# Performance work log

Measured on AMD Instinct MI355X. Metric: run time of the kernel, lower is better.

## Reference

```python
import jax, jax.numpy as jnp
import numpy as np

N, E, F_IN, H, C, K = 50000, 800000, 100, 128, 10, 5


def setup_inputs() -> dict:
    key = jax.random.key(0)
    ks = jax.random.split(key, 8)
    x = jax.random.normal(ks[0], (N, F_IN), jnp.float32)
    edge_index = jax.random.randint(ks[1], (2, E), 0, N, dtype=jnp.int64)
    edge_weight = jax.random.uniform(ks[2], (E,), jnp.float32)
    # Hop-wise linear weights: PyG TAGConv holds K+1 bias-free Linears per layer
    W1 = jax.random.normal(ks[3], (K + 1, F_IN, H), jnp.float32) / np.sqrt(F_IN).astype(np.float32)
    b1 = jnp.zeros((H,), jnp.float32)
    W2 = jax.random.normal(ks[4], (K + 1, H, H), jnp.float32) / np.sqrt(H).astype(np.float32)
    b2 = jnp.zeros((H,), jnp.float32)
    W3 = jax.random.normal(ks[5], (K + 1, H, C), jnp.float32) / np.sqrt(H).astype(np.float32)
    b3 = jnp.zeros((C,), jnp.float32)
    return dict(x=x, edge_index=edge_index, edge_weight=edge_weight,
                W1=W1, b1=b1, W2=W2, b2=b2, W3=W3, b3=b3)


def _gcn_norm(row, col, edge_weight, num_nodes):
    # symmetric normalization D^{-1/2} A D^{-1/2}, no self loops (TAGConv default)
    deg = jax.ops.segment_sum(edge_weight, col, num_segments=num_nodes)
    dis = jnp.where(deg > 0, jax.lax.rsqrt(jnp.maximum(deg, 1e-12)), 0.0)
    return dis[row] * edge_weight * dis[col]


def _tagconv(x, row, col, norm, W, b, num_nodes):
    # out = sum_{k=0..K} (A_norm^k x) @ W[k] + b
    out = x @ W[0] + b
    h = x
    for k in range(1, W.shape[0]):
        msg = norm[:, None] * h[row]                       # [E, d] gather
        h = jax.ops.segment_sum(msg, col, num_segments=num_nodes)  # scatter-add
        out = out + h @ W[k]
    return out


def reference(x, edge_index, edge_weight, W1, b1, W2, b2, W3, b3):
    row, col = edge_index[0], edge_index[1]
    norm = _gcn_norm(row, col, edge_weight, N)
    h = jax.nn.elu(_tagconv(x, row, col, norm, W1, b1, N))
    h = jax.nn.elu(_tagconv(h, row, col, norm, W2, b2, N))
    return _tagconv(h, row, col, norm, W3, b3, N)
```

## Files before the change

kernel.cpp:

```cpp
#include <hip/hip_runtime.h>
#include <cstdint>
#include <cstddef>

#define N_NODES 50000
#define N_EDGES 800000
#define F_IN_D 100
#define HDIM 128
#define CDIM 10
#define NCH ((N_NODES + 255) / 256)
#define NLINES 64

typedef unsigned short ushortT;

__device__ __forceinline__ float bf2f(unsigned int b16) {
  return __uint_as_float(b16 << 16);
}
__device__ __forceinline__ unsigned int f2bf(float f) {
  unsigned int u = __float_as_uint(f);
  unsigned int r = u + 0x7FFFu + ((u >> 16) & 1u);
  return r >> 16;
}

struct Args {
  const float* x; const int* ei; const float* ew;
  const float* W1; const float* b1;
  const float* W2; const float* b2;
  const float* W3; const float* b3;
  float* out;
  ushortT* Yall;
  char* A; char* B;
  ushortT* C; ushortT* D;
  int* ptrA; int* pos; int* srcs; float* wsrt;
  int* row32; int* col32; float* deg; float* dis; int* cnt; int* part;
  int* lines;
  int* gbl;
};

__device__ __forceinline__ void gbar(int* lines, int* gbl, int round, int gdim) {
  __syncthreads();
  if (threadIdx.x == 0) {
    __threadfence();
    const int perLine = gdim / NLINES;
    int old = atomicAdd(&lines[(blockIdx.x & (NLINES - 1)) * 32], 1);
    if (old == round * perLine - 1) atomicAdd(gbl, 1);
    while (__hip_atomic_load(gbl, __ATOMIC_ACQUIRE, __HIP_MEMORY_SCOPE_AGENT) < round * NLINES)
      __builtin_amdgcn_s_sleep(8);
    __threadfence();
  }
  __syncthreads();
}

template <int K_DIM, int BMODE, bool XBF, bool OUTBF>
__device__ __forceinline__ void gemm_tile(const void* __restrict__ Xv, const float* __restrict__ W,
                                          const float* __restrict__ bias, bool addb,
                                          void* __restrict__ outv, int ostride, int tile,
                                          float (&xt)[32][68], float (&bt)[32][64]) {
  const int tid = threadIdx.x;
  const int tx = tid & 15;
  const int ty = tid >> 4;
  int n0, c0;
  if (BMODE == 0) { n0 = (tile >> 1) * 64; c0 = (tile & 1) * 64; }
  else            { n0 = tile * 64;        c0 = 0; }
  float acc[4][4];
#pragma unroll
  for (int i = 0; i < 4; ++i)
#pragma unroll
    for (int j = 0; j < 4; ++j) acc[i][j] = 0.f;

  for (int k0 = 0; k0 < K_DIM; k0 += 32) {
#pragma unroll
    for (int i = 0; i < 8; ++i) {
      int idx = tid + i * 256;
      int nl = idx >> 5, kl = idx & 31;
      int nn = n0 + nl, kg = k0 + kl;
      float v = 0.f;
      if (nn < N_NODES && kg < K_DIM) {
        if (XBF) v = bf2f(((const ushortT*)Xv)[(size_t)nn * K_DIM + kg]);
        else     v = ((const float*)Xv)[(size_t)nn * K_DIM + kg];
      }
      xt[kl][nl] = v;
    }
#pragma unroll
    for (int i = 0; i < 8; ++i) {
      int idx = tid + i * 256;
      int kl = idx >> 6, cl = idx & 63;
      int kg = k0 + kl;
      float v = 0.f;
      if (BMODE == 0) {
        if (kg < K_DIM) v = W[(size_t)kg * 128 + c0 + cl];
      } else {
        if (kg < K_DIM && cl < 6 * CDIM)
          v = W[(size_t)(cl / CDIM) * (K_DIM * CDIM) + (size_t)kg * CDIM + (cl % CDIM)];
      }
      bt[kl][cl] = v;
    }
    __syncthreads();
#pragma unroll
    for (int kk = 0; kk < 32; ++kk) {
      float4 xv = *(const float4*)&xt[kk][tx * 4];
      float4 bv = *(const float4*)&bt[kk][ty * 4];
      acc[0][0] += xv.x * bv.x; acc[0][1] += xv.x * bv.y; acc[0][2] += xv.x * bv.z; acc[0][3] += xv.x * bv.w;
      acc[1][0] += xv.y * bv.x; acc[1][1] += xv.y * bv.y; acc[1][2] += xv.y * bv.z; acc[1][3] += xv.y * bv.w;
      acc[2][0] += xv.z * bv.x; acc[2][1] += xv.z * bv.y; acc[2][2] += xv.z * bv.z; acc[2][3] += xv.z * bv.w;
      acc[3][0] += xv.w * bv.x; acc[3][1] += xv.w * bv.y; acc[3][2] += xv.w * bv.z; acc[3][3] += xv.w * bv.w;
    }
    __syncthreads();
  }
#pragma unroll
  for (int i = 0; i < 4; ++i) {
    int nn = n0 + tx * 4 + i;
    if (nn >= N_NODES) continue;
#pragma unroll
    for (int j = 0; j < 4; ++j) {
      int c = c0 + ty * 4 + j;
      if (addb) {
        if (BMODE == 0) acc[i][j] += bias[c];
        else if (c < CDIM) acc[i][j] += bias[c];
      }
    }
    if (OUTBF) {
      uint2 o;
      o.x = f2bf(acc[i][0]) | (f2bf(acc[i][1]) << 16);
      o.y = f2bf(acc[i][2]) | (f2bf(acc[i][3]) << 16);
      *(uint2*)&((ushortT*)outv)[(size_t)nn * ostride + c0 + ty * 4] = o;
    } else {
#pragma unroll
      for (int j = 0; j < 4; ++j)
        ((float*)outv)[(size_t)nn * ostride + c0 + ty * 4 + j] = acc[i][j];
    }
  }
}

template <bool ELU>
__device__ __forceinline__ void hopb_phase(const uint2* __restrict__ P2, int pstr,
                                           const uint2* __restrict__ Y2, int ystr,
                                           const int* __restrict__ ptr, const int* __restrict__ srcs,
                                           const float* __restrict__ w, uint2* __restrict__ Q2) {
  const int hw = threadIdx.x >> 5;
  const int f4 = threadIdx.x & 31;
  for (int node = blockIdx.x * 8 + hw; node < N_NODES; node += gridDim.x * 8) {
    const int b = ptr[node], e = ptr[node + 1];
    uint2 yv = Y2[(size_t)node * ystr + f4];
    float a0 = bf2f(yv.x & 0xFFFFu), a1 = bf2f(yv.x >> 16);
    float a2 = bf2f(yv.y & 0xFFFFu), a3 = bf2f(yv.y >> 16);
    int j = b;
    for (; j + 7 < e; j += 8) {
      int s0 = srcs[j], s1 = srcs[j + 1], s2 = srcs[j + 2], s3 = srcs[j + 3];
      int s4 = srcs[j + 4], s5 = srcs[j + 5], s6 = srcs[j + 6], s7 = srcs[j + 7];
      float w0 = w[j], w1 = w[j + 1], w2 = w[j + 2], w3 = w[j + 3];
      float w4 = w[j + 4], w5 = w[j + 5], w6 = w[j + 6], w7 = w[j + 7];
      uint2 v0 = P2[(size_t)s0 * pstr + f4];
      uint2 v1 = P2[(size_t)s1 * pstr + f4];
      uint2 v2 = P2[(size_t)s2 * pstr + f4];
      uint2 v3 = P2[(size_t)s3 * pstr + f4];
      uint2 v4 = P2[(size_t)s4 * pstr + f4];
      uint2 v5 = P2[(size_t)s5 * pstr + f4];
      uint2 v6 = P2[(size_t)s6 * pstr + f4];
      uint2 v7 = P2[(size_t)s7 * pstr + f4];
      a0 += w0 * bf2f(v0.x & 0xFFFFu) + w1 * bf2f(v1.x & 0xFFFFu) + w2 * bf2f(v2.x & 0xFFFFu) + w3 * bf2f(v3.x & 0xFFFFu)
          + w4 * bf2f(v4.x & 0xFFFFu) + w5 * bf2f(v5.x & 0xFFFFu) + w6 * bf2f(v6.x & 0xFFFFu) + w7 * bf2f(v7.x & 0xFFFFu);
      a1 += w0 * bf2f(v0.x >> 16) + w1 * bf2f(v1.x >> 16) + w2 * bf2f(v2.x >> 16) + w3 * bf2f(v3.x >> 16)
          + w4 * bf2f(v4.x >> 16) + w5 * bf2f(v5.x >> 16) + w6 * bf2f(v6.x >> 16) + w7 * bf2f(v7.x >> 16);
      a2 += w0 * bf2f(v0.y & 0xFFFFu) + w1 * bf2f(v1.y & 0xFFFFu) + w2 * bf2f(v2.y & 0xFFFFu) + w3 * bf2f(v3.y & 0xFFFFu)
          + w4 * bf2f(v4.y & 0xFFFFu) + w5 * bf2f(v5.y & 0xFFFFu) + w6 * bf2f(v6.y & 0xFFFFu) + w7 * bf2f(v7.y & 0xFFFFu);
      a3 += w0 * bf2f(v0.y >> 16) + w1 * bf2f(v1.y >> 16) + w2 * bf2f(v2.y >> 16) + w3 * bf2f(v3.y >> 16)
          + w4 * bf2f(v4.y >> 16) + w5 * bf2f(v5.y >> 16) + w6 * bf2f(v6.y >> 16) + w7 * bf2f(v7.y >> 16);
    }
    for (; j + 1 < e; j += 2) {
      int s0 = srcs[j], s1 = srcs[j + 1];
      float w0 = w[j], w1 = w[j + 1];
      uint2 v0 = P2[(size_t)s0 * pstr + f4];
      uint2 v1 = P2[(size_t)s1 * pstr + f4];
      a0 += w0 * bf2f(v0.x & 0xFFFFu) + w1 * bf2f(v1.x & 0xFFFFu);
      a1 += w0 * bf2f(v0.x >> 16)     + w1 * bf2f(v1.x >> 16);
      a2 += w0 * bf2f(v0.y & 0xFFFFu) + w1 * bf2f(v1.y & 0xFFFFu);
      a3 += w0 * bf2f(v0.y >> 16)     + w1 * bf2f(v1.y >> 16);
    }
    if (j < e) {
      float w0 = w[j];
      uint2 v0 = P2[(size_t)srcs[j] * pstr + f4];
      a0 += w0 * bf2f(v0.x & 0xFFFFu);
      a1 += w0 * bf2f(v0.x >> 16);
      a2 += w0 * bf2f(v0.y & 0xFFFFu);
      a3 += w0 * bf2f(v0.y >> 16);
    }
    if (ELU) {
      a0 = a0 > 0.f ? a0 : expm1f(a0);
      a1 = a1 > 0.f ? a1 : expm1f(a1);
      a2 = a2 > 0.f ? a2 : expm1f(a2);
      a3 = a3 > 0.f ? a3 : expm1f(a3);
    }
    uint2 o;
    o.x = f2bf(a0) | (f2bf(a1) << 16);
    o.y = f2bf(a2) | (f2bf(a3) << 16);
    Q2[(size_t)node * 32 + f4] = o;
  }
}

__device__ __forceinline__ void hop10_phase(const float* __restrict__ z, int zStride, int zOff,
                                            const float* __restrict__ ybuf, int yOff,
                                            const int* __restrict__ ptr, const int* __restrict__ srcs,
                                            const float* __restrict__ wsrt, float* __restrict__ outp) {
  const int lane = threadIdx.x & 63;
  const int wid = threadIdx.x >> 6;
  const int sub = lane >> 4;
  const int f = lane & 15;
  for (int node = blockIdx.x * 4 + wid; node < N_NODES; node += gridDim.x * 4) {
    const int b = ptr[node], e = ptr[node + 1];
    const int len = e - b;
    const int js = b + (len * sub) / 4;
    const int je = b + (len * (sub + 1)) / 4;
    float acc = 0.f;
    if (f < CDIM) {
      if (sub == 0) acc = ybuf[(size_t)node * 64 + yOff + f];
      int j = js;
      for (; j + 1 < je; j += 2) {
        int s0 = srcs[j], s1 = srcs[j + 1];
        float w0 = wsrt[j], w1 = wsrt[j + 1];
        acc += w0 * z[(size_t)s0 * zStride + zOff + f] + w1 * z[(size_t)s1 * zStride + zOff + f];
      }
      if (j < je) acc += wsrt[j] * z[(size_t)srcs[j] * zStride + zOff + f];
    }
    acc += __shfl_xor(acc, 16);
    acc += __shfl_xor(acc, 32);
    if (sub == 0 && f < CDIM) outp[(size_t)node * CDIM + f] = acc;
  }
}

__global__ __launch_bounds__(256, 4) void mega_kernel(Args a) {
  __shared__ float xt[32][68];
  __shared__ float bt[32][64];
  __shared__ int sdi[256];
  const int tid = threadIdx.x;
  const int gtid = blockIdx.x * blockDim.x + tid;
  const int gstride = gridDim.x * blockDim.x;
  const int gdim = gridDim.x;
  const int TG0 = ((N_NODES + 63) / 64) * 2;
  const int TG1 = (N_NODES + 63) / 64;
  int nb = 0;

  {
    bool is64 = true;
    for (int i = 0; i < 32; ++i) if (a.ei[2 * i + 1] != 0) is64 = false;
    for (int e = gtid; e < N_EDGES; e += gstride) {
      int r, c;
      if (is64) { r = a.ei[2 * e]; c = a.ei[2 * (N_EDGES + e)]; }
      else      { r = a.ei[e];     c = a.ei[N_EDGES + e]; }
      a.row32[e] = r; a.col32[e] = c;
      atomicAdd(&a.deg[c], a.ew[e]);
      atomicAdd(&a.cnt[c], 1);
    }
  }
  for (int job = blockIdx.x; job < 6 * TG0; job += gdim) {
    int k = job / TG0, t = job % TG0;
    gemm_tile<F_IN_D, 0, false, true>(a.x, a.W1 + (size_t)k * F_IN_D * 128, a.b1, k == 0,
                                      a.Yall + k * 128, 768, t, xt, bt);
  }
  gbar(a.lines, a.gbl, ++nb, gdim);

  for (int i = gtid; i < N_NODES; i += gstride) {
    float d = a.deg[i];
    a.dis[i] = d > 0.f ? rsqrtf(fmaxf(d, 1e-12f)) : 0.f;
  }
  for (int c = blockIdx.x; c < NCH; c += gdim) {
    int i = c * 256 + tid;
    sdi[tid] = (i < N_NODES) ? a.cnt[i] : 0;
    __syncthreads();
    for (int s = 128; s > 0; s >>= 1) { if (tid < s) sdi[tid] += sdi[tid + s]; __syncthreads(); }
    if (tid == 0) a.part[c] = sdi[0];
    __syncthreads();
  }
  gbar(a.lines, a.gbl, ++nb, gdim);

  if (blockIdx.x == 0) {
    int v = (tid < NCH) ? a.part[tid] : 0;
    sdi[tid] = v;
    __syncthreads();
    for (int o = 1; o < 256; o <<= 1) {
      int t2 = (tid >= o) ? sdi[tid - o] : 0;
      __syncthreads();
      sdi[tid] += t2;
      __syncthreads();
    }
    if (tid < NCH) a.part[tid] = sdi[tid] - v;
    if (tid == 255) a.ptrA[N_NODES] = sdi[255];
  }
  gbar(a.lines, a.gbl, ++nb, gdim);

  for (int c = blockIdx.x; c < NCH; c += gdim) {
    int i = c * 256 + tid;
    int v = (i < N_NODES) ? a.cnt[i] : 0;
    sdi[tid] = v;
    __syncthreads();
    for (int o = 1; o < 256; o <<= 1) {
      int t2 = (tid >= o) ? sdi[tid - o] : 0;
      __syncthreads();
      sdi[tid] += t2;
      __syncthreads();
    }
    if (i < N_NODES) { int p = a.part[c] + sdi[tid] - v; a.ptrA[i] = p; a.pos[i] = p; }
    __syncthreads();
  }
  gbar(a.lines, a.gbl, ++nb, gdim);

  for (int e = gtid; e < N_EDGES; e += gstride) {
    int r = a.row32[e], c = a.col32[e];
    int slot = atomicAdd(&a.pos[c], 1);
    a.srcs[slot] = r;
    a.wsrt[slot] = a.dis[r] * a.ew[e] * a.dis[c];
  }
  gbar(a.lines, a.gbl, ++nb, gdim);

  const uint2* Y2 = (const uint2*)a.Yall;
  uint2* A2 = (uint2*)a.A; uint2* B2 = (uint2*)a.B;
  uint2* C2 = (uint2*)a.C; uint2* D2 = (uint2*)a.D;

  hopb_phase<false>(Y2 + 5 * 32, 192, Y2 + 4 * 32, 192, a.ptrA, a.srcs, a.wsrt, A2);
  gbar(a.lines, a.gbl, ++nb, gdim);
  hopb_phase<false>(A2, 32, Y2 + 3 * 32, 192, a.ptrA, a.srcs, a.wsrt, B2);
  gbar(a.lines, a.gbl, ++nb, gdim);
  hopb_phase<false>(B2, 32, Y2 + 2 * 32, 192, a.ptrA, a.srcs, a.wsrt, A2);
  gbar(a.lines, a.gbl, ++nb, gdim);
  hopb_phase<false>(A2, 32, Y2 + 1 * 32, 192, a.ptrA, a.srcs, a.wsrt, B2);
  gbar(a.lines, a.gbl, ++nb, gdim);
  hopb_phase<true>(B2, 32, Y2 + 0 * 32, 192, a.ptrA, a.srcs, a.wsrt, C2);
  gbar(a.lines, a.gbl, ++nb, gdim);

  for (int job = blockIdx.x; job < 6 * TG0; job += gdim) {
    int k = job / TG0, t = job % TG0;
    gemm_tile<HDIM, 0, true, true>(a.C, a.W2 + (size_t)k * HDIM * 128, a.b2, k == 0,
                                   a.Yall + k * 128, 768, t, xt, bt);
  }
  gbar(a.lines, a.gbl, ++nb, gdim);
  hopb_phase<false>(Y2 + 5 * 32, 192, Y2 + 4 * 32, 192, a.ptrA, a.srcs, a.wsrt, A2);
  gbar(a.lines, a.gbl, ++nb, gdim);
  hopb_phase<false>(A2, 32, Y2 + 3 * 32, 192, a.ptrA, a.srcs, a.wsrt, B2);
  gbar(a.lines, a.gbl, ++nb, gdim);
  hopb_phase<false>(B2, 32, Y2 + 2 * 32, 192, a.ptrA, a.srcs, a.wsrt, A2);
  gbar(a.lines, a.gbl, ++nb, gdim);
  hopb_phase<false>(A2, 32, Y2 + 1 * 32, 192, a.ptrA, a.srcs, a.wsrt, B2);
  gbar(a.lines, a.gbl, ++nb, gdim);
  hopb_phase<true>(B2, 32, Y2 + 0 * 32, 192, a.ptrA, a.srcs, a.wsrt, D2);
  gbar(a.lines, a.gbl, ++nb, gdim);

  float* ybuf = (float*)a.A;
  float* z0 = (float*)a.B;
  float* z1 = (float*)(a.B + (size_t)N_NODES * 16 * 4);
  for (int t = blockIdx.x; t < TG1; t += gdim)
    gemm_tile<HDIM, 1, true, false>(a.D, a.W3, a.b3, true, ybuf, 64, t, xt, bt);
  gbar(a.lines, a.gbl, ++nb, gdim);
  hop10_phase(ybuf, 64, 50, ybuf, 40, a.ptrA, a.srcs, a.wsrt, z0); gbar(a.lines, a.gbl, ++nb, gdim);
  hop10_phase(z0, 10, 0, ybuf, 30, a.ptrA, a.srcs, a.wsrt, z1); gbar(a.lines, a.gbl, ++nb, gdim);
  hop10_phase(z1, 10, 0, ybuf, 20, a.ptrA, a.srcs, a.wsrt, z0); gbar(a.lines, a.gbl, ++nb, gdim);
  hop10_phase(z0, 10, 0, ybuf, 10, a.ptrA, a.srcs, a.wsrt, z1); gbar(a.lines, a.gbl, ++nb, gdim);
  hop10_phase(z1, 10, 0, ybuf, 0, a.ptrA, a.srcs, a.wsrt, a.out);
}


extern "C" void kernel_launch(void* const* d_in, const int* in_sizes, int n_in,
                              void* d_out, int out_size, void* d_ws, size_t ws_size,
                              hipStream_t stream) {
  Args a;
  a.x  = (const float*)d_in[0];
  a.ei = (const int*)d_in[1];
  a.ew = (const float*)d_in[2];
  a.W1 = (const float*)d_in[3];
  a.b1 = (const float*)d_in[4];
  a.W2 = (const float*)d_in[5];
  a.b2 = (const float*)d_in[6];
  a.W3 = (const float*)d_in[7];
  a.b3 = (const float*)d_in[8];
  a.out = (float*)d_out;

  const int N = N_NODES, E = N_EDGES;
  char* base = (char*)d_ws;
  size_t off = 0;
  auto alloc = [&](size_t bytes) -> char* {
    char* p = base + off;
    off += (bytes + 255) & ~(size_t)255;
    return p;
  };
  a.Yall = (ushortT*)alloc((size_t)N * 768 * 2);
  a.A = alloc((size_t)N * 256);
  a.B = alloc((size_t)N * 256);
  a.C = (ushortT*)alloc((size_t)N * 128 * 2);
  a.D = (ushortT*)alloc((size_t)N * 128 * 2);
  a.ptrA = (int*)alloc((size_t)(N + 1) * 4);
  a.pos  = (int*)alloc((size_t)N * 4);
  a.srcs = (int*)alloc((size_t)E * 4);
  a.wsrt = (float*)alloc((size_t)E * 4);
  a.lines = (int*)alloc(NLINES * 32 * 4);
  a.gbl   = (int*)alloc(256);

  char* t = a.A;
  a.row32 = (int*)t;            t += (size_t)E * 4;
  a.col32 = (int*)t;            t += (size_t)E * 4;
  a.deg   = (float*)t;          t += (size_t)N * 4;
  a.dis   = (float*)t;          t += (size_t)N * 4;
  a.cnt   = (int*)t;            t += (size_t)N * 4;
  a.part  = (int*)t;            t += 2048 * 4;

  hipMemsetAsync(a.lines, 0, NLINES * 32 * 4, stream);
  hipMemsetAsync(a.gbl, 0, 256, stream);
  hipMemsetAsync(a.deg, 0, (size_t)N * 4, stream);
  hipMemsetAsync(a.cnt, 0, (size_t)N * 4, stream);

  int occ = 0;
  hipOccupancyMaxActiveBlocksPerMultiprocessor(&occ, (const void*)mega_kernel, 256, 0);
  if (occ < 1) occ = 1;
  int grid = occ * 256;
  if (grid > 2048) grid = 2048;
  if (grid < 64) grid = 64;
  grid &= ~(NLINES - 1);

  void* args[] = { &a };
  hipLaunchCooperativeKernel((const void*)mega_kernel, dim3(grid), dim3(256), args, 0, stream);

  (void)in_sizes; (void)n_in; (void)out_size; (void)ws_size;
}
```

Before: 4.201 ms.

## Use bf16 MFMA for dense hop GEMM tiles and cap cooperative grid

Replaces the FP32 scalar-FMA GEMM tile with a bf16 MFMA 16x16x32 version. The full 64x128 input tile and the transposed weight tile are staged once in shared memory as bf16, then each wave computes 16 rows by 64 columns. The goal is to cut the dense-projection compute cost. The cooperative grid is also capped at 1024 blocks, which reduces barrier participants but may lower occupancy in the gather phases. FP32 inputs of the first layer are now rounded to bf16, which reduces precision, and the output stores are scalar instead of vectorized.

```diff
diff --git a/kernel.cpp b/kernel.cpp
--- a/kernel.cpp
+++ b/kernel.cpp
@@ -11,6 +11,8 @@
 #define NLINES 64
 
 typedef unsigned short ushortT;
+typedef __attribute__((ext_vector_type(8))) short bf16x8;
+typedef __attribute__((ext_vector_type(4))) float f32x4;
 
 __device__ __forceinline__ float bf2f(unsigned int b16) {
   return __uint_as_float(b16 << 16);
@@ -32,8 +34,7 @@
   ushortT* C; ushortT* D;
   int* ptrA; int* pos; int* srcs; float* wsrt;
   int* row32; int* col32; float* deg; float* dis; int* cnt; int* part;
-  int* lines;
-  int* gbl;
+  int* lines; int* gbl;
 };
 
 __device__ __forceinline__ void gbar(int* lines, int* gbl, int round, int gdim) {
@@ -54,79 +55,79 @@
 __device__ __forceinline__ void gemm_tile(const void* __restrict__ Xv, const float* __restrict__ W,
                                           const float* __restrict__ bias, bool addb,
                                           void* __restrict__ outv, int ostride, int tile,
-                                          float (&xt)[32][68], float (&bt)[32][64]) {
+                                          ushortT* xb, ushortT* wb) {
   const int tid = threadIdx.x;
-  const int tx = tid & 15;
-  const int ty = tid >> 4;
   int n0, c0;
   if (BMODE == 0) { n0 = (tile >> 1) * 64; c0 = (tile & 1) * 64; }
   else            { n0 = tile * 64;        c0 = 0; }
-  float acc[4][4];
+
 #pragma unroll
-  for (int i = 0; i < 4; ++i)
+  for (int i = 0; i < 32; ++i) {
+    int idx = tid + i * 256;
+    int nl = idx >> 7, kl = idx & 127;
+    int nn = n0 + nl;
+    ushortT v = 0;
+    if (nn < N_NODES && kl < K_DIM) {
+      if (XBF) v = ((const ushortT*)Xv)[(size_t)nn * K_DIM + kl];
+      else     v = (ushortT)f2bf(((const float*)Xv)[(size_t)nn * K_DIM + kl]);
+    }
+    xb[nl * 128 + kl] = v;
+  }
 #pragma unroll
-    for (int j = 0; j < 4; ++j) acc[i][j] = 0.f;
-
-  for (int k0 = 0; k0 < K_DIM; k0 += 32) {
+  for (int i = 0; i < 32; ++i) {
+    int idx = tid + i * 256;
+    int kl = idx >> 6, cl = idx & 63;
+    float v = 0.f;
+    if (BMODE == 0) {
+      if (kl < K_DIM) v = W[(size_t)kl * 128 + c0 + cl];
+    } else {
+      if (kl < K_DIM && cl < 6 * CDIM)
+        v = W[(size_t)(cl / CDIM) * (K_DIM * CDIM) + (size_t)kl * CDIM + (cl % CDIM)];
+    }
+    wb[cl * 128 + kl] = (ushortT)f2bf(v);
+  }
+  __syncthreads();
+
+  const int wv = tid >> 6;
+  const int l = tid & 63;
+  const int lr = l & 15;
+  const int lk = (l >> 4) * 8;
+
+  f32x4 acc0 = {0.f, 0.f, 0.f, 0.f}, acc1 = acc0, acc2 = acc0, acc3 = acc0;
 #pragma unroll
-    for (int i = 0; i < 8; ++i) {
-      int idx = tid + i * 256;
-      int nl = idx >> 5, kl = idx & 31;
-      int nn = n0 + nl, kg = k0 + kl;
-      float v = 0.f;
-      if (nn < N_NODES && kg < K_DIM) {
-        if (XBF) v = bf2f(((const ushortT*)Xv)[(size_t)nn * K_DIM + kg]);
-        else     v = ((const float*)Xv)[(size_t)nn * K_DIM + kg];
-      }
-      xt[kl][nl] = v;
-    }
+  for (int kc = 0; kc < 128; kc += 32) {
+    bf16x8 af = *(const bf16x8*)&xb[(wv * 16 + lr) * 128 + kc + lk];
+    bf16x8 b0 = *(const bf16x8*)&wb[(0 + lr) * 128 + kc + lk];
+    bf16x8 b1 = *(const bf16x8*)&wb[(16 + lr) * 128 + kc + lk];
+    bf16x8 b2 = *(const bf16x8*)&wb[(32 + lr) * 128 + kc + lk];
+    bf16x8 b3 = *(const bf16x8*)&wb[(48 + lr) * 128 + kc + lk];
+    acc0 = __builtin_amdgcn_mfma_f32_16x16x32_bf16(af, b0, acc0, 0, 0, 0);
+    acc1 = __builtin_amdgcn_mfma_f32_16x16x32_bf16(af, b1, acc1, 0, 0, 0);
+    acc2 = __builtin_amdgcn_mfma_f32_16x16x32_bf16(af, b2, acc2, 0, 0, 0);
+    acc3 = __builtin_amdgcn_mfma_f32_16x16x32_bf16(af, b3, acc3, 0, 0, 0);
+  }
+  __syncthreads();
+
+  const int rbase = n0 + wv * 16 + (l >> 4) * 4;
+  const int NCOL = (BMODE == 0) ? 64 : 6 * CDIM;
 #pragma unroll
-    for (int i = 0; i < 8; ++i) {
-      int idx = tid + i * 256;
-      int kl = idx >> 6, cl = idx & 63;
-      int kg = k0 + kl;
-      float v = 0.f;
-      if (BMODE == 0) {
-        if (kg < K_DIM) v = W[(size_t)kg * 128 + c0 + cl];
-      } else {
-        if (kg < K_DIM && cl < 6 * CDIM)
-          v = W[(size_t)(cl / CDIM) * (K_DIM * CDIM) + (size_t)kg * CDIM + (cl % CDIM)];
-      }
-      bt[kl][cl] = v;
-    }
-    __syncthreads();
-#pragma unroll
-    for (int kk = 0; kk < 32; ++kk) {
-      float4 xv = *(const float4*)&xt[kk][tx * 4];
-      float4 bv = *(const float4*)&bt[kk][ty * 4];
-      acc[0][0] += xv.x * bv.x; acc[0][1] += xv.x * bv.y; acc[0][2] += xv.x * bv.z; acc[0][3] += xv.x * bv.w;
-      acc[1][0] += xv.y * bv.x; acc[1][1] += xv.y * bv.y; acc[1][2] += xv.y * bv.z; acc[1][3] += xv.y * bv.w;
-      acc[2][0] += xv.z * bv.x; acc[2][1] += xv.z * bv.y; acc[2][2] += xv.z * bv.z; acc[2][3] += xv.z * bv.w;
-      acc[3][0] += xv.w * bv.x; acc[3][1] += xv.w * bv.y; acc[3][2] += xv.w * bv.z; acc[3][3] += xv.w * bv.w;
-    }
-    __syncthreads();
-  }
-#pragma unroll
-  for (int i = 0; i < 4; ++i) {
-    int nn = n0 + tx * 4 + i;
-    if (nn >= N_NODES) continue;
+  for (int ct = 0; ct < 4; ++ct) {
+    f32x4 av = (ct == 0) ? acc0 : (ct == 1) ? acc1 : (ct == 2) ? acc2 : acc3;
+    int cc = ct * 16 + lr;
+    if (cc >= NCOL) continue;
+    int gc = c0 + cc;
+    float badd = 0.f;
+    if (addb) {
+      if (BMODE == 0) badd = bias[gc];
+      else if (gc < CDIM) badd = bias[gc];
+    }
 #pragma unroll
     for (int j = 0; j < 4; ++j) {
-      int c = c0 + ty * 4 + j;
-      if (addb) {
-        if (BMODE == 0) acc[i][j] += bias[c];
-        else if (c < CDIM) acc[i][j] += bias[c];
-      }
-    }
-    if (OUTBF) {
-      uint2 o;
-      o.x = f2bf(acc[i][0]) | (f2bf(acc[i][1]) << 16);
-      o.y = f2bf(acc[i][2]) | (f2bf(acc[i][3]) << 16);
-      *(uint2*)&((ushortT*)outv)[(size_t)nn * ostride + c0 + ty * 4] = o;
-    } else {
-#pragma unroll
-      for (int j = 0; j < 4; ++j)
-        ((float*)outv)[(size_t)nn * ostride + c0 + ty * 4 + j] = acc[i][j];
+      int rr = rbase + j;
+      if (rr >= N_NODES) continue;
+      float r = av[j] + badd;
+      if (OUTBF) ((ushortT*)outv)[(size_t)rr * ostride + gc] = (ushortT)f2bf(r);
+      else       ((float*)outv)[(size_t)rr * ostride + gc] = r;
     }
   }
 }
@@ -228,9 +229,10 @@
 }
 
 __global__ __launch_bounds__(256, 4) void mega_kernel(Args a) {
-  __shared__ float xt[32][68];
-  __shared__ float bt[32][64];
-  __shared__ int sdi[256];
+  __shared__ ushortT smem[16384];
+  ushortT* xb = smem;
+  ushortT* wb = smem + 64 * 128;
+  int* sdi = (int*)smem;
   const int tid = threadIdx.x;
   const int gtid = blockIdx.x * blockDim.x + tid;
   const int gstride = gridDim.x * blockDim.x;
@@ -251,10 +253,11 @@
       atomicAdd(&a.cnt[c], 1);
     }
   }
+  __syncthreads();
   for (int job = blockIdx.x; job < 6 * TG0; job += gdim) {
     int k = job / TG0, t = job % TG0;
     gemm_tile<F_IN_D, 0, false, true>(a.x, a.W1 + (size_t)k * F_IN_D * 128, a.b1, k == 0,
-                                      a.Yall + k * 128, 768, t, xt, bt);
+                                      a.Yall + k * 128, 768, t, xb, wb);
   }
   gbar(a.lines, a.gbl, ++nb, gdim);
 
@@ -329,7 +332,7 @@
   for (int job = blockIdx.x; job < 6 * TG0; job += gdim) {
     int k = job / TG0, t = job % TG0;
     gemm_tile<HDIM, 0, true, true>(a.C, a.W2 + (size_t)k * HDIM * 128, a.b2, k == 0,
-                                   a.Yall + k * 128, 768, t, xt, bt);
+                                   a.Yall + k * 128, 768, t, xb, wb);
   }
   gbar(a.lines, a.gbl, ++nb, gdim);
   hopb_phase<false>(Y2 + 5 * 32, 192, Y2 + 4 * 32, 192, a.ptrA, a.srcs, a.wsrt, A2);
@@ -347,7 +350,7 @@
   float* z0 = (float*)a.B;
   float* z1 = (float*)(a.B + (size_t)N_NODES * 16 * 4);
   for (int t = blockIdx.x; t < TG1; t += gdim)
-    gemm_tile<HDIM, 1, true, false>(a.D, a.W3, a.b3, true, ybuf, 64, t, xt, bt);
+    gemm_tile<HDIM, 1, true, false>(a.D, a.W3, a.b3, true, ybuf, 64, t, xb, wb);
   gbar(a.lines, a.gbl, ++nb, gdim);
   hop10_phase(ybuf, 64, 50, ybuf, 40, a.ptrA, a.srcs, a.wsrt, z0); gbar(a.lines, a.gbl, ++nb, gdim);
   hop10_phase(z0, 10, 0, ybuf, 30, a.ptrA, a.srcs, a.wsrt, z1); gbar(a.lines, a.gbl, ++nb, gdim);
@@ -409,9 +412,9 @@
   hipOccupancyMaxActiveBlocksPerMultiprocessor(&occ, (const void*)mega_kernel, 256, 0);
   if (occ < 1) occ = 1;
   int grid = occ * 256;
-  if (grid > 2048) grid = 2048;
-  if (grid < 64) grid = 64;
+  if (grid > 1024) grid = 1024;
   grid &= ~(NLINES - 1);
+  if (grid < NLINES) grid = NLINES;
 
   void* args[] = { &a };
   hipLaunchCooperativeKernel((const void*)mega_kernel, dim3(grid), dim3(256), args, 0, stream);
```

New measurement: 3.492 ms. 1.2x faster.
